# Optimization experiments

Hardware: AMD Instinct MI355X
Metric: run time of the kernel (lower is better)

The kernel has to match this reference:

```python
import jax, jax.numpy as jnp
import numpy as np

TEMP = 0.07
POS_WINDOW = 2
EPS = 1e-8
NEG = -1e9  # finite large-negative for masking (safe under vjp)


def _l2norm(x):
    # matches F.normalize(dim=-1) with eps=1e-12
    n = jnp.sqrt(jnp.sum(x * x, axis=-1, keepdims=True))
    return x / jnp.maximum(n, 1e-12)


def setup_inputs() -> dict:
    key = jax.random.key(0)
    k1, k2, k3, k4, k5 = jax.random.split(key, 5)
    B, T, D = 32, 1024, 256
    eeg_enc = jax.random.normal(k1, (B, T, D), dtype=jnp.float32)
    eye_enc = jax.random.normal(k2, (B, T, D), dtype=jnp.float32)
    mask = jax.random.randint(k3, (B, T), 0, 2, dtype=jnp.int32)
    W_eeg = jax.random.normal(k4, (D, D), dtype=jnp.float32) / np.sqrt(D)
    W_eye = jax.random.normal(k5, (D, D), dtype=jnp.float32) / np.sqrt(D)
    return {"eeg_enc": eeg_enc, "eye_enc": eye_enc, "mask": mask,
            "W_eeg": W_eeg, "W_eye": W_eye}


def reference(eeg_enc, eye_enc, mask, W_eeg, W_eye):
    B, T, D = eeg_enc.shape
    valid = mask > 0  # (B,T)
    # nn.Linear(bias=False): x @ W.T, then L2-normalize
    e = _l2norm(jnp.einsum('btd,ed->bte', eeg_enc, W_eeg))
    v = _l2norm(jnp.einsum('btd,ed->bte', eye_enc, W_eye))
    sims = jnp.einsum('bid,bjd->bij', e, v) / TEMP  # (B,T,T)
    # rank of each valid step within the compressed (gathered) ordering
    rank = jnp.cumsum(valid.astype(jnp.int32), axis=-1) - 1  # (B,T)
    band = jnp.abs(rank[:, :, None] - rank[:, None, :]) <= POS_WINDOW
    pair = valid[:, :, None] & valid[:, None, :]  # both steps valid
    pos = pair & band
    # per-row max over positive (banded) entries
    pos_scores = jnp.max(jnp.where(pos, sims, NEG), axis=-1)  # (B,T)
    # logsumexp over valid columns (the gathered sims row)
    lse = jax.nn.logsumexp(jnp.where(valid[:, None, :], sims, NEG), axis=-1)
    row_loss = -(pos_scores - lse)  # (B,T)
    Tv = jnp.sum(valid, axis=-1)  # (B,)
    per_b = jnp.sum(jnp.where(valid, row_loss, 0.0), axis=-1) / jnp.maximum(Tv, 1)
    per_b = jnp.where(Tv >= 2, per_b, 0.0)  # skip samples with <2 valid steps
    return jnp.sum(per_b) / (B + EPS)
```

## Files before the change

### kernel.cpp

```cpp
#include <hip/hip_runtime.h>
#include <hip/hip_bf16.h>

typedef __attribute__((ext_vector_type(8))) short bf16x8;
typedef __attribute__((ext_vector_type(4))) float f32x4;

#define INVT (1.0f/0.07f)

static __device__ __forceinline__ short f2bf(float f){
    unsigned int u = __float_as_uint(f);
    unsigned int r = (u + 0x7fffu + ((u >> 16) & 1u)) >> 16;
    return (short)r;
}
static __device__ __forceinline__ float bf2f(short s){
    return __uint_as_float(((unsigned int)(unsigned short)s) << 16);
}

__global__ __launch_bounds__(256) void prep_kernel(const float* __restrict__ Weeg,
                                                   const float* __restrict__ Weye,
                                                   const int* __restrict__ mask,
                                                   short* __restrict__ Wout,
                                                   int* __restrict__ rank,
                                                   int* __restrict__ idx,
                                                   int* __restrict__ Tv,
                                                   float* __restrict__ cb){
    __shared__ int ssum[256];
    int tid = threadIdx.x;
    if (blockIdx.x < 512){
        int i = blockIdx.x * 256 + tid;
        float v = (i < 65536) ? Weeg[i] : Weye[i - 65536];
        Wout[i] = f2bf(v);
        return;
    }
    int b = blockIdx.x - 512;
    int local[4]; int s = 0;
    #pragma unroll
    for (int q = 0; q < 4; ++q){
        int t = tid*4 + q;
        local[q] = (mask[b*1024 + t] > 0) ? 1 : 0;
        s += local[q];
    }
    ssum[tid] = s;
    __syncthreads();
    for (int off = 1; off < 256; off <<= 1){
        int add = (tid >= off) ? ssum[tid - off] : 0;
        __syncthreads();
        ssum[tid] += add;
        __syncthreads();
    }
    int run = ssum[tid] - s;
    #pragma unroll
    for (int q = 0; q < 4; ++q){
        int t = tid*4 + q;
        int g = b*1024 + t;
        run += local[q];
        rank[g] = run - 1;
        cb[g]   = local[q] ? 0.0f : -1e9f;
        if (local[q]) idx[b*1024 + run - 1] = t;
    }
    if (tid == 255) Tv[b] = ssum[255];
}

__global__ __launch_bounds__(256, 3) void proj_kernel(const float* __restrict__ Aeeg,
                                                      const float* __restrict__ Aeye,
                                                      const short* __restrict__ Wbf,
                                                      short* __restrict__ Eout,
                                                      short* __restrict__ Vout){
    __shared__ short sW[64 * 264];
    int sel = blockIdx.y;
    const float* A   = sel ? Aeye : Aeeg;
    const short* W   = Wbf + sel * 65536;
    short*       Out = sel ? Vout : Eout;

    int tid = threadIdx.x;
    int w = tid >> 6, lane = tid & 63;
    int l15 = lane & 15, lq = lane >> 4;
    int kb  = lq * 8;
    int row0 = blockIdx.x * 64;

    bf16x8 xf[8];
    {
        const float* ap = A + (size_t)(row0 + w*16 + l15) * 256 + kb;
        #pragma unroll
        for (int g = 0; g < 8; ++g){
            float4 x0 = *(const float4*)(ap + g*32);
            float4 x1 = *(const float4*)(ap + g*32 + 4);
            bf16x8 t;
            t[0]=f2bf(x0.x); t[1]=f2bf(x0.y); t[2]=f2bf(x0.z); t[3]=f2bf(x0.w);
            t[4]=f2bf(x1.x); t[5]=f2bf(x1.y); t[6]=f2bf(x1.z); t[7]=f2bf(x1.w);
            xf[g] = t;
        }
    }

    f32x4 acc[16];
    #pragma unroll
    for (int q = 0; q < 16; ++q) acc[q] = (f32x4){0.f,0.f,0.f,0.f};

    #pragma unroll
    for (int pass = 0; pass < 4; ++pass){
        if (pass) __syncthreads();
        #pragma unroll
        for (int p = 0; p < 8; ++p){
            int flat = p*2048 + tid*8;
            int r = flat >> 8, c = flat & 255;
            *(int4*)&sW[r*264 + c] = *(const int4*)(W + (size_t)(pass*64 + r)*256 + c);
        }
        __syncthreads();
        #pragma unroll
        for (int nt = 0; nt < 4; ++nt){
            f32x4 c = acc[pass*4 + nt];
            const short* wp = &sW[(nt*16 + l15) * 264 + kb];
            #pragma unroll
            for (int g = 0; g < 8; ++g){
                bf16x8 wf = *(const bf16x8*)(wp + g*32);
                c = __builtin_amdgcn_mfma_f32_16x16x32_bf16(wf, xf[g], c, 0, 0, 0);
            }
            acc[pass*4 + nt] = c;
        }
    }

    float ss = 0.f;
    #pragma unroll
    for (int q = 0; q < 16; ++q){
        #pragma unroll
        for (int r = 0; r < 4; ++r){ float x = acc[q][r]; ss += x*x; }
    }
    ss += __shfl_xor(ss, 16);
    ss += __shfl_xor(ss, 32);
    float scale = 1.0f / fmaxf(sqrtf(ss), 1e-12f);

    short* op = Out + (size_t)(row0 + w*16 + l15) * 256 + lq*4;
    #pragma unroll
    for (int q = 0; q < 16; ++q){
        short4 pk;
        pk.x = f2bf(acc[q][0] * scale);
        pk.y = f2bf(acc[q][1] * scale);
        pk.z = f2bf(acc[q][2] * scale);
        pk.w = f2bf(acc[q][3] * scale);
        *(short4*)(op + ((q >> 2) * 64 + (q & 3) * 16)) = pk;
    }
}

__global__ __launch_bounds__(256, 2) void loss_kernel(const short* __restrict__ E,
                                                      const short* __restrict__ V,
                                                      const float* __restrict__ cb,
                                                      float* __restrict__ psum){
    __shared__ short sV[64 * 264];
    __shared__ float sCb[256];

    int ib = blockIdx.x;
    int js = blockIdx.y;
    int b  = blockIdx.z;
    int i0 = ib * 256;

    int tid = threadIdx.x;
    int w = tid >> 6, lane = tid & 63;
    int l15 = lane & 15, lq = lane >> 4;
    int kb = lq * 8;

    sCb[tid] = cb[b*1024 + js*256 + tid];

    bf16x8 af[4][8];
    {
        const short* ep = E + ((size_t)b*1024 + i0 + w*64 + l15) * 256 + kb;
        #pragma unroll
        for (int s = 0; s < 4; ++s){
            #pragma unroll
            for (int g = 0; g < 8; ++g)
                af[s][g] = *(const bf16x8*)(ep + s*16*256 + g*32);
        }
    }

    float ls[4][4];
    #pragma unroll
    for (int s = 0; s < 4; ++s)
        #pragma unroll
        for (int r = 0; r < 4; ++r) ls[s][r] = 0.f;

    const short* vb = V + ((size_t)b*1024 + js*256) * 256;

    #pragma unroll
    for (int jc = 0; jc < 4; ++jc){
        __syncthreads();
        #pragma unroll
        for (int p = 0; p < 8; ++p){
            int flat = p*2048 + tid*8;
            int r = flat >> 8, c = flat & 255;
            *(int4*)&sV[r*264 + c] = *(const int4*)(vb + (size_t)(jc*64 + r)*256 + c);
        }
        __syncthreads();

        #pragma unroll
        for (int jt = 0; jt < 4; ++jt){
            f32x4 c0 = {0.f,0.f,0.f,0.f};
            f32x4 c1 = {0.f,0.f,0.f,0.f};
            f32x4 c2 = {0.f,0.f,0.f,0.f};
            f32x4 c3 = {0.f,0.f,0.f,0.f};
            const short* vp = &sV[(jt*16 + l15) * 264 + kb];
            #pragma unroll
            for (int g = 0; g < 8; ++g){
                bf16x8 bf = *(const bf16x8*)(vp + g*32);
                c0 = __builtin_amdgcn_mfma_f32_16x16x32_bf16(af[0][g], bf, c0, 0, 0, 0);
                c1 = __builtin_amdgcn_mfma_f32_16x16x32_bf16(af[1][g], bf, c1, 0, 0, 0);
                c2 = __builtin_amdgcn_mfma_f32_16x16x32_bf16(af[2][g], bf, c2, 0, 0, 0);
                c3 = __builtin_amdgcn_mfma_f32_16x16x32_bf16(af[3][g], bf, c3, 0, 0, 0);
            }
            float cbj = sCb[jc*64 + jt*16 + l15];
            #pragma unroll
            for (int r = 0; r < 4; ++r){
                ls[0][r] += __expf(fmaf(c0[r], INVT, cbj));
                ls[1][r] += __expf(fmaf(c1[r], INVT, cbj));
                ls[2][r] += __expf(fmaf(c2[r], INVT, cbj));
                ls[3][r] += __expf(fmaf(c3[r], INVT, cbj));
            }
        }
    }

    #pragma unroll
    for (int s = 0; s < 4; ++s){
        #pragma unroll
        for (int r = 0; r < 4; ++r){
            #pragma unroll
            for (int m = 1; m < 16; m <<= 1)
                ls[s][r] += __shfl_xor(ls[s][r], m);
        }
    }
    if (l15 == 0){
        float* pp = psum + (((size_t)(b*4 + js)) << 10);
        int ibase = i0 + w*64 + lq*4;
        #pragma unroll
        for (int s = 0; s < 4; ++s){
            #pragma unroll
            for (int r = 0; r < 4; ++r)
                pp[ibase + s*16 + r] = ls[s][r];
        }
    }
}

__global__ __launch_bounds__(256) void pos_kernel(const short* __restrict__ E,
                                                  const short* __restrict__ V,
                                                  const int* __restrict__ mask,
                                                  const int* __restrict__ rank,
                                                  const int* __restrict__ idx,
                                                  const int* __restrict__ Tv,
                                                  float* __restrict__ pmax){
    int tid = threadIdx.x;
    int gl  = tid & 15;
    int rf  = (blockIdx.x * 256 + tid) >> 4;
    int b   = rf >> 10;
    if (mask[rf] <= 0) return;

    int ri = rank[rf];
    int tv = Tv[b];
    int lo = ri - 2; if (lo < 0) lo = 0;
    int hi = ri + 2; if (hi > tv - 1) hi = tv - 1;

    const short* epp = E + (size_t)rf * 256 + gl * 16;
    float ev[16];
    {
        bf16x8 e0 = *(const bf16x8*)epp;
        bf16x8 e1 = *(const bf16x8*)(epp + 8);
        #pragma unroll
        for (int k = 0; k < 8; ++k){ ev[k] = bf2f(e0[k]); ev[8+k] = bf2f(e1[k]); }
    }
    float pm = -1e30f;
    for (int r = lo; r <= hi; ++r){
        int j = idx[b*1024 + r];
        const short* vpp = V + ((size_t)(b*1024) + j) * 256 + gl * 16;
        bf16x8 v0 = *(const bf16x8*)vpp;
        bf16x8 v1 = *(const bf16x8*)(vpp + 8);
        float s = 0.f;
        #pragma unroll
        for (int k = 0; k < 8; ++k){
            s = fmaf(ev[k],   bf2f(v0[k]), s);
            s = fmaf(ev[8+k], bf2f(v1[k]), s);
        }
        s += __shfl_xor(s, 1);
        s += __shfl_xor(s, 2);
        s += __shfl_xor(s, 4);
        s += __shfl_xor(s, 8);
        pm = fmaxf(pm, s);
    }
    if (gl == 0) pmax[rf] = pm * INVT;
}

__global__ __launch_bounds__(256) void reduce_kernel(const float* __restrict__ psum,
                                                     const float* __restrict__ pmax,
                                                     const int* __restrict__ mask,
                                                     const int* __restrict__ Tv,
                                                     float* __restrict__ per_b){
    __shared__ float sred[4];
    int b = blockIdx.x, tid = threadIdx.x;
    float a = 0.f;
    const float* pp = psum + (((size_t)(b*4)) << 10);
    #pragma unroll
    for (int q = 0; q < 4; ++q){
        int i = q*256 + tid;
        int g = b*1024 + i;
        if (mask[g] > 0){
            float ps = pp[i] + pp[i + 1024] + pp[i + 2048] + pp[i + 3072];
            a += logf(ps) - pmax[g];
        }
    }
    #pragma unroll
    for (int m = 1; m < 64; m <<= 1) a += __shfl_xor(a, m);
    if ((tid & 63) == 0) sred[tid >> 6] = a;
    __syncthreads();
    if (tid == 0){
        float t = sred[0] + sred[1] + sred[2] + sred[3];
        int tv = Tv[b];
        per_b[b] = (tv >= 2) ? t / (float)tv : 0.f;
    }
}

__global__ void final_kernel(const float* __restrict__ per_b,
                             float* __restrict__ out){
    int tid = threadIdx.x;
    float v = (tid < 32) ? per_b[tid] : 0.f;
    #pragma unroll
    for (int m = 1; m < 64; m <<= 1) v += __shfl_xor(v, m);
    if (tid == 0) out[0] = v / 32.0f;
}

extern "C" void kernel_launch(void* const* d_in, const int* in_sizes, int n_in,
                              void* d_out, int out_size, void* d_ws, size_t ws_size,
                              hipStream_t stream) {
    const float* eeg  = (const float*)d_in[0];
    const float* eye  = (const float*)d_in[1];
    const int*   mask = (const int*)d_in[2];
    const float* Weeg = (const float*)d_in[3];
    const float* Weye = (const float*)d_in[4];
    float* out = (float*)d_out;

    char* ws = (char*)d_ws;
    short* e_bf  = (short*)(ws);
    short* v_bf  = (short*)(ws + 16777216);
    short* wbf   = (short*)(ws + 33554432);
    int*   rank  = (int*)  (ws + 33816576);
    int*   idx   = (int*)  (ws + 33947648);
    float* cb    = (float*)(ws + 34078720);
    float* psum  = (float*)(ws + 34209792);
    float* pmax  = (float*)(ws + 34734080);
    int*   Tv    = (int*)  (ws + 34865152);
    float* per_b = (float*)(ws + 34865280);

    prep_kernel<<<544, 256, 0, stream>>>(Weeg, Weye, mask, wbf, rank, idx, Tv, cb);
    proj_kernel<<<dim3(512, 2), 256, 0, stream>>>(eeg, eye, wbf, e_bf, v_bf);
    loss_kernel<<<dim3(4, 4, 32), 256, 0, stream>>>(e_bf, v_bf, cb, psum);
    pos_kernel<<<2048, 256, 0, stream>>>(e_bf, v_bf, mask, rank, idx, Tv, pmax);
    reduce_kernel<<<32, 256, 0, stream>>>(psum, pmax, mask, Tv, per_b);
    final_kernel<<<1, 64, 0, stream>>>(per_b, out);
}
```

Before: 177.5 us.

## Retile loss GEMM into 128x128 blocks with K-chunked LDS staging

The similarity/logsumexp kernel is reorganised. Each block now computes a 128x128 tile per batch, with a 2x2 warp grid. E and V are both staged through LDS in 64-wide K chunks using global_load_lds direct loads, instead of holding a 256-row E slab in registers and streaming V. This cuts per-thread register pressure, allowing occupancy 4, and launches 2048 blocks instead of 512. The cost is 16 partial sums per row instead of 4, a larger psum workspace, and more syncs and shared-memory traffic per MFMA.

```diff
diff --git a/kernel.cpp b/kernel.cpp
--- a/kernel.cpp
+++ b/kernel.cpp
@@ -13,6 +13,12 @@
 }
 static __device__ __forceinline__ float bf2f(short s){
     return __uint_as_float(((unsigned int)(unsigned short)s) << 16);
+}
+
+static __device__ __forceinline__ void gld16(const void* g, void* l){
+    __builtin_amdgcn_global_load_lds(
+        (const __attribute__((address_space(1))) unsigned int*)g,
+        (__attribute__((address_space(3))) unsigned int*)l, 16, 0, 0);
 }
 
 __global__ __launch_bounds__(256) void prep_kernel(const float* __restrict__ Weeg,
@@ -140,98 +146,97 @@
     }
 }
 
-__global__ __launch_bounds__(256, 2) void loss_kernel(const short* __restrict__ E,
+__global__ __launch_bounds__(256, 4) void loss_kernel(const short* __restrict__ E,
                                                       const short* __restrict__ V,
                                                       const float* __restrict__ cb,
                                                       float* __restrict__ psum){
-    __shared__ short sV[64 * 264];
-    __shared__ float sCb[256];
-
-    int ib = blockIdx.x;
-    int js = blockIdx.y;
+    __shared__ short sE[128 * 64];
+    __shared__ short sV[128 * 64];
+
+    int i0 = blockIdx.x * 128;
+    int j0 = blockIdx.y * 128;
     int b  = blockIdx.z;
-    int i0 = ib * 256;
 
     int tid = threadIdx.x;
     int w = tid >> 6, lane = tid & 63;
+    int wi = w >> 1, wj = w & 1;
     int l15 = lane & 15, lq = lane >> 4;
     int kb = lq * 8;
 
-    sCb[tid] = cb[b*1024 + js*256 + tid];
-
-    bf16x8 af[4][8];
-    {
-        const short* ep = E + ((size_t)b*1024 + i0 + w*64 + l15) * 256 + kb;
-        #pragma unroll
-        for (int s = 0; s < 4; ++s){
-            #pragma unroll
-            for (int g = 0; g < 8; ++g)
-                af[s][g] = *(const bf16x8*)(ep + s*16*256 + g*32);
+    const short* Eg = E + ((size_t)b*1024 + i0 + w*32 + (lane>>3))*256 + (lane&7)*8;
+    const short* Vg = V + ((size_t)b*1024 + j0 + w*32 + (lane>>3))*256 + (lane&7)*8;
+    short* sEw = &sE[(w*32)*64];
+    short* sVw = &sV[(w*32)*64];
+
+    float cbv[4];
+    #pragma unroll
+    for (int jj = 0; jj < 4; ++jj)
+        cbv[jj] = cb[b*1024 + j0 + wj*64 + jj*16 + l15];
+
+    f32x4 acc[4][4];
+    #pragma unroll
+    for (int ii = 0; ii < 4; ++ii)
+        #pragma unroll
+        for (int jj = 0; jj < 4; ++jj) acc[ii][jj] = (f32x4){0.f,0.f,0.f,0.f};
+
+    #pragma unroll
+    for (int kc = 0; kc < 4; ++kc){
+        __syncthreads();
+        #pragma unroll
+        for (int p = 0; p < 4; ++p){
+            gld16(Eg + kc*64 + p*2048, sEw + p*512);
+            gld16(Vg + kc*64 + p*2048, sVw + p*512);
+        }
+        __syncthreads();
+
+        #pragma unroll
+        for (int ks = 0; ks < 2; ++ks){
+            bf16x8 af[4], bf[4];
+            #pragma unroll
+            for (int t = 0; t < 4; ++t){
+                af[t] = *(const bf16x8*)&sE[(wi*64 + t*16 + l15)*64 + ks*32 + kb];
+                bf[t] = *(const bf16x8*)&sV[(wj*64 + t*16 + l15)*64 + ks*32 + kb];
+            }
+            #pragma unroll
+            for (int ii = 0; ii < 4; ++ii)
+                #pragma unroll
+                for (int jj = 0; jj < 4; ++jj)
+                    acc[ii][jj] = __builtin_amdgcn_mfma_f32_16x16x32_bf16(af[ii], bf[jj], acc[ii][jj], 0, 0, 0);
         }
     }
 
     float ls[4][4];
     #pragma unroll
-    for (int s = 0; s < 4; ++s)
-        #pragma unroll
-        for (int r = 0; r < 4; ++r) ls[s][r] = 0.f;
-
-    const short* vb = V + ((size_t)b*1024 + js*256) * 256;
-
-    #pragma unroll
-    for (int jc = 0; jc < 4; ++jc){
-        __syncthreads();
-        #pragma unroll
-        for (int p = 0; p < 8; ++p){
-            int flat = p*2048 + tid*8;
-            int r = flat >> 8, c = flat & 255;
-            *(int4*)&sV[r*264 + c] = *(const int4*)(vb + (size_t)(jc*64 + r)*256 + c);
-        }
-        __syncthreads();
-
-        #pragma unroll
-        for (int jt = 0; jt < 4; ++jt){
-            f32x4 c0 = {0.f,0.f,0.f,0.f};
-            f32x4 c1 = {0.f,0.f,0.f,0.f};
-            f32x4 c2 = {0.f,0.f,0.f,0.f};
-            f32x4 c3 = {0.f,0.f,0.f,0.f};
-            const short* vp = &sV[(jt*16 + l15) * 264 + kb];
-            #pragma unroll
-            for (int g = 0; g < 8; ++g){
-                bf16x8 bf = *(const bf16x8*)(vp + g*32);
-                c0 = __builtin_amdgcn_mfma_f32_16x16x32_bf16(af[0][g], bf, c0, 0, 0, 0);
-                c1 = __builtin_amdgcn_mfma_f32_16x16x32_bf16(af[1][g], bf, c1, 0, 0, 0);
-                c2 = __builtin_amdgcn_mfma_f32_16x16x32_bf16(af[2][g], bf, c2, 0, 0, 0);
-                c3 = __builtin_amdgcn_mfma_f32_16x16x32_bf16(af[3][g], bf, c3, 0, 0, 0);
-            }
-            float cbj = sCb[jc*64 + jt*16 + l15];
-            #pragma unroll
-            for (int r = 0; r < 4; ++r){
-                ls[0][r] += __expf(fmaf(c0[r], INVT, cbj));
-                ls[1][r] += __expf(fmaf(c1[r], INVT, cbj));
-                ls[2][r] += __expf(fmaf(c2[r], INVT, cbj));
-                ls[3][r] += __expf(fmaf(c3[r], INVT, cbj));
-            }
-        }
-    }
-
-    #pragma unroll
-    for (int s = 0; s < 4; ++s){
+    for (int ii = 0; ii < 4; ++ii){
         #pragma unroll
         for (int r = 0; r < 4; ++r){
-            #pragma unroll
-            for (int m = 1; m < 16; m <<= 1)
-                ls[s][r] += __shfl_xor(ls[s][r], m);
+            float s = 0.f;
+            #pragma unroll
+            for (int jj = 0; jj < 4; ++jj)
+                s += __expf(fmaf(acc[ii][jj][r], INVT, cbv[jj]));
+            ls[ii][r] = s;
+        }
+    }
+    #pragma unroll
+    for (int ii = 0; ii < 4; ++ii){
+        #pragma unroll
+        for (int r = 0; r < 4; ++r){
+            float v = ls[ii][r];
+            v += __shfl_xor(v, 1);
+            v += __shfl_xor(v, 2);
+            v += __shfl_xor(v, 4);
+            v += __shfl_xor(v, 8);
+            ls[ii][r] = v;
         }
     }
     if (l15 == 0){
-        float* pp = psum + (((size_t)(b*4 + js)) << 10);
-        int ibase = i0 + w*64 + lq*4;
-        #pragma unroll
-        for (int s = 0; s < 4; ++s){
+        float* pp = psum + (((size_t)(b*16 + blockIdx.y*2 + wj)) << 10);
+        int ibase = i0 + wi*64 + lq*4;
+        #pragma unroll
+        for (int ii = 0; ii < 4; ++ii){
             #pragma unroll
             for (int r = 0; r < 4; ++r)
-                pp[ibase + s*16 + r] = ls[s][r];
+                pp[ibase + ii*16 + r] = ls[ii][r];
         }
     }
 }
@@ -291,13 +296,15 @@
     __shared__ float sred[4];
     int b = blockIdx.x, tid = threadIdx.x;
     float a = 0.f;
-    const float* pp = psum + (((size_t)(b*4)) << 10);
+    const float* pp = psum + ((size_t)b << 14);
     #pragma unroll
     for (int q = 0; q < 4; ++q){
         int i = q*256 + tid;
         int g = b*1024 + i;
         if (mask[g] > 0){
-            float ps = pp[i] + pp[i + 1024] + pp[i + 2048] + pp[i + 3072];
+            float ps = 0.f;
+            #pragma unroll
+            for (int s = 0; s < 16; ++s) ps += pp[i + (s << 10)];
             a += logf(ps) - pmax[g];
         }
     }
@@ -339,13 +346,13 @@
     int*   idx   = (int*)  (ws + 33947648);
     float* cb    = (float*)(ws + 34078720);
     float* psum  = (float*)(ws + 34209792);
-    float* pmax  = (float*)(ws + 34734080);
-    int*   Tv    = (int*)  (ws + 34865152);
-    float* per_b = (float*)(ws + 34865280);
+    float* pmax  = (float*)(ws + 36306944);
+    int*   Tv    = (int*)  (ws + 36438016);
+    float* per_b = (float*)(ws + 36438144);
 
     prep_kernel<<<544, 256, 0, stream>>>(Weeg, Weye, mask, wbf, rank, idx, Tv, cb);
     proj_kernel<<<dim3(512, 2), 256, 0, stream>>>(eeg, eye, wbf, e_bf, v_bf);
-    loss_kernel<<<dim3(4, 4, 32), 256, 0, stream>>>(e_bf, v_bf, cb, psum);
+    loss_kernel<<<dim3(8, 8, 32), 256, 0, stream>>>(e_bf, v_bf, cb, psum);
     pos_kernel<<<2048, 256, 0, stream>>>(e_bf, v_bf, mask, rank, idx, Tv, pmax);
     reduce_kernel<<<32, 256, 0, stream>>>(psum, pmax, mask, Tv, per_b);
     final_kernel<<<1, 64, 0, stream>>>(per_b, out);
```

After: 171.6 us. -3.3%, faster.
